# Kernel optimization log

Measured on AMD Instinct MI355X. Metric: run time of the kernel, lower is better.

## Reference

```python
import jax, jax.numpy as jnp
import numpy as np

N1, E1 = 50000, 400000   # drug graph nodes/edges
N2, E2 = 50000, 400000   # second-branch nodes/edges
G = 256                   # number of graphs in the batch
F1, F2 = 93, 43           # node feature dims


def setup_inputs() -> dict:
    key = jax.random.key(0)
    ks = jax.random.split(key, 40)
    rn = lambda k, s, sc=0.05: jax.random.normal(k, s, dtype=jnp.float32) * sc
    inp = {}
    inp["data"] = 0  # unused placeholder arg in the original forward
    inp["x"] = jax.random.normal(ks[0], (N1, F1), dtype=jnp.float32)
    inp["edge_index"] = jax.random.randint(ks[1], (2, E1), 0, N1)
    inp["batch"] = jnp.sort(jax.random.randint(ks[2], (N1,), 0, G))
    inp["a"] = jax.random.normal(ks[3], (N2, F2), dtype=jnp.float32)
    inp["edge"] = jax.random.randint(ks[4], (2, E2), 0, N2)
    inp["c"] = jnp.sort(jax.random.randint(ks[5], (N2,), 0, G))
    # GINConv linear weights (x @ W + b convention)
    inp["W1"] = rn(ks[6], (F1, F1));        inp["b1"] = rn(ks[7], (F1,))
    inp["W2"] = rn(ks[8], (F1, F1 * 10));   inp["b2"] = rn(ks[9], (F1 * 10,))
    inp["W3"] = rn(ks[10], (F2, F2));       inp["b3"] = rn(ks[11], (F2,))
    inp["W4"] = rn(ks[12], (F2, F2 * 10));  inp["b4"] = rn(ks[13], (F2 * 10,))
    # fc_g: 1860 -> 1024 -> 512 ; fc_g1: 860 -> 1024 -> 512
    inp["fcg_w1"] = rn(ks[14], (F1 * 10 * 2, 1024)); inp["fcg_b1"] = rn(ks[15], (1024,))
    inp["fcg_w2"] = rn(ks[16], (1024, 512));         inp["fcg_b2"] = rn(ks[17], (512,))
    inp["fcg1_w1"] = rn(ks[18], (F2 * 10 * 2, 1024)); inp["fcg1_b1"] = rn(ks[19], (1024,))
    inp["fcg1_w2"] = rn(ks[20], (1024, 512));         inp["fcg1_b2"] = rn(ks[21], (512,))
    # fc_final / fc_final1: 512 -> 256 -> 1
    inp["ff_w1"] = rn(ks[22], (512, 256)); inp["ff_b1"] = rn(ks[23], (256,))
    inp["ff_w2"] = rn(ks[24], (256, 1));   inp["ff_b2"] = rn(ks[25], (1,))
    inp["ff1_w1"] = rn(ks[26], (512, 256)); inp["ff1_b1"] = rn(ks[27], (256,))
    inp["ff1_w2"] = rn(ks[28], (256, 1));   inp["ff1_b2"] = rn(ks[29], (1,))
    return inp


def _gin(h, ei, W, b):
    # PyG GINConv(eps=0): Linear(x_i + sum_{j->i} x_j)
    agg = jax.ops.segment_sum(h[ei[0]], ei[1], num_segments=h.shape[0])
    return (h + agg) @ W + b


def _pool(h, seg):
    # concat(global_max_pool, global_mean_pool) per graph -> [G, 2*d]
    s = jax.ops.segment_sum(h, seg, num_segments=G)
    cnt = jax.ops.segment_sum(jnp.ones((h.shape[0], 1), h.dtype), seg, num_segments=G)
    mean = s / jnp.maximum(cnt, 1.0)
    mx = jax.ops.segment_max(h, seg, num_segments=G)
    mx = jnp.where(jnp.isfinite(mx), mx, 0.0)
    return jnp.concatenate([mx, mean], axis=1)


def reference(data, x, edge_index, batch, a, edge, c,
              W1, b1, W2, b2, W3, b3, W4, b4,
              fcg_w1, fcg_b1, fcg_w2, fcg_b2,
              fcg1_w1, fcg1_b1, fcg1_w2, fcg1_b2,
              ff_w1, ff_b1, ff_w2, ff_b2,
              ff1_w1, ff1_b1, ff1_w2, ff1_b2):
    relu = jax.nn.relu
    # branch 1 (93-dim features)
    h = relu(_gin(x, edge_index, W1, b1))
    h = relu(_gin(h, edge_index, W2, b2))          # [N1, 930]
    p = _pool(h, batch)                             # [G, 1860]
    x_g = relu(p @ fcg_w1 + fcg_b1) @ fcg_w2 + fcg_b2   # [G, 512] (dropout = identity at eval)
    z = relu(x_g @ ff_w1 + ff_b1) @ ff_w2 + ff_b2        # [G, 1]
    # branch 2 (43-dim features)
    h1 = relu(_gin(a, edge, W3, b3))
    h1 = relu(_gin(h1, edge, W4, b4))               # [N2, 430]
    p1 = _pool(h1, c)                                # [G, 860]
    x_g1 = relu(p1 @ fcg1_w1 + fcg1_b1) @ fcg1_w2 + fcg1_b2  # [G, 512]
    z1 = relu(x_g1 @ ff1_w1 + ff1_b1) @ ff1_w2 + ff1_b2       # [G, 1]
    return (z, x_g, x_g1, z1)
```

## Files before the change

### kernel.cpp

```cpp
#include <hip/hip_runtime.h>


static constexpr int NG  = 256;
static constexpr int CHK = 4096;

typedef short  short8  __attribute__((ext_vector_type(8)));
typedef float  floatx4 __attribute__((ext_vector_type(4)));

__device__ __forceinline__ short f2bf(float f) {
    unsigned u = __float_as_uint(f);
    u += 0x7fff + ((u >> 16) & 1);
    return (short)(u >> 16);
}
__device__ __forceinline__ float bf_lo(unsigned u) { return __uint_as_float(u << 16); }
__device__ __forceinline__ float bf_hi(unsigned u) { return __uint_as_float(u & 0xffff0000u); }

static inline int cdiv(int a, int b) { return (a + b - 1) / b; }

__global__ void offs_both_kernel(const int* __restrict__ s1, int n1, int* __restrict__ o1,
                                 const int* __restrict__ s2, int n2, int* __restrict__ o2) {
    int t = blockIdx.x * 256 + threadIdx.x;
    int br = t >> 9;
    int g = t & 511;
    if (br > 1 || g > NG) return;
    const int* seg = br ? s2 : s1;
    int N = br ? n2 : n1;
    int* offs = br ? o2 : o1;
    int lo = 0, hi = N;
    while (lo < hi) {
        int mid = (lo + hi) >> 1;
        if (seg[mid] < g) lo = mid + 1; else hi = mid;
    }
    offs[g] = lo;
}

__device__ __forceinline__ void deg_win_dev(const int* __restrict__ ei, int E, int N,
                                            int* __restrict__ deg, int bid) {
    int win = bid & 7, chunk = bid >> 3;
    int e0 = chunk * CHK;
    int e1 = e0 + CHK; if (e1 > E) e1 = E;
    int wlo = (int)((long)win * N / 8);
    int whi = (int)((long)(win + 1) * N / 8);
    for (int e = e0 + threadIdx.x; e < e1; e += 256) {
        int dst = ei[E + e];
        if (dst >= wlo && dst < whi) atomicAdd(&deg[dst], 1);
    }
}

__global__ __launch_bounds__(256) void deg_win_both_kernel(
        const int* ei1, int E1, int N1, int* d1, int nblk1,
        const int* ei2, int E2, int N2, int* d2) {
    int bid = blockIdx.x;
    if (bid < nblk1) deg_win_dev(ei1, E1, N1, d1, bid);
    else             deg_win_dev(ei2, E2, N2, d2, bid - nblk1);
}

__global__ __launch_bounds__(256) void scan1_both_kernel(
        const int* __restrict__ d1, int N1, int* __restrict__ x1, int* __restrict__ bs1, int nb1,
        const int* __restrict__ d2, int N2, int* __restrict__ x2, int* __restrict__ bs2) {
    __shared__ int sh[256];
    const int* deg; int* excl; int* bsum; int N; int blk;
    if ((int)blockIdx.x < nb1) { deg = d1; excl = x1; bsum = bs1; N = N1; blk = blockIdx.x; }
    else { deg = d2; excl = x2; bsum = bs2; N = N2; blk = blockIdx.x - nb1; }
    int base = blk * 1024;
    int t = threadIdx.x;
    int v[4];
    int s = 0;
    #pragma unroll
    for (int i = 0; i < 4; ++i) {
        int idx = base + t * 4 + i;
        v[i] = s;
        s += (idx < N) ? deg[idx] : 0;
    }
    sh[t] = s;
    __syncthreads();
    for (int off = 1; off < 256; off <<= 1) {
        int xv = (t >= off) ? sh[t - off] : 0;
        __syncthreads();
        sh[t] += xv;
        __syncthreads();
    }
    int texcl = (t > 0) ? sh[t - 1] : 0;
    #pragma unroll
    for (int i = 0; i < 4; ++i) {
        int idx = base + t * 4 + i;
        if (idx < N) excl[idx] = texcl + v[i];
    }
    if (t == 255) bsum[blk] = sh[255];
}

__global__ void scan2_both_kernel(int* __restrict__ b1, int nb1,
                                  int* __restrict__ b2, int nb2) {
    if (threadIdx.x) return;
    int* b = blockIdx.x ? b2 : b1;
    int nb = blockIdx.x ? nb2 : nb1;
    int acc = 0;
    for (int i = 0; i < nb; ++i) { int t = b[i]; b[i] = acc; acc += t; }
}

__global__ void scan3_both_kernel(int* __restrict__ x1, const int* __restrict__ bs1,
                                  int* __restrict__ c1, int N1, int Ev1,
                                  int* __restrict__ x2, const int* __restrict__ bs2,
                                  int* __restrict__ c2, int N2, int Ev2, int nc1) {
    int bid = blockIdx.x;
    int* excl; const int* bsum; int* cur; int N, E, i;
    if (bid < nc1) { i = bid * 256 + threadIdx.x; excl = x1; bsum = bs1; cur = c1; N = N1; E = Ev1; }
    else { i = (bid - nc1) * 256 + threadIdx.x; excl = x2; bsum = bs2; cur = c2; N = N2; E = Ev2; }
    if (i < N) {
        int v = excl[i] + bsum[i >> 10];
        excl[i] = v;
        cur[i] = v;
    }
    if (i == 0) excl[N] = E;
}

__device__ __forceinline__ void fill_win_dev(const int* __restrict__ ei, int E, int N,
                                             int* __restrict__ cursor, int* __restrict__ csr,
                                             int bid) {
    int win = bid & 7, chunk = bid >> 3;
    int e0 = chunk * CHK;
    int e1 = e0 + CHK; if (e1 > E) e1 = E;
    int wlo = (int)((long)win * N / 8);
    int whi = (int)((long)(win + 1) * N / 8);
    for (int e = e0 + threadIdx.x; e < e1; e += 256) {
        int dst = ei[E + e];
        if (dst >= wlo && dst < whi) {
            int pos = atomicAdd(&cursor[dst], 1);
            csr[pos] = ei[e];
        }
    }
}

__global__ __launch_bounds__(256) void fill_win_both_kernel(
        const int* ei1, int E1, int N1, int* c1, int* s1, int nblk1,
        const int* ei2, int E2, int N2, int* c2, int* s2) {
    int bid = blockIdx.x;
    if (bid < nblk1) fill_win_dev(ei1, E1, N1, c1, s1, bid);
    else             fill_win_dev(ei2, E2, N2, c2, s2, bid - nblk1);
}

struct RJob { const float* W; short* Wb; int K, Nsrc, Ndst, KP; };
struct RJobs10 { RJob j[10]; };

__global__ __launch_bounds__(256) void repack_all_kernel(RJobs10 jobs) {
    __shared__ __align__(16) short sh[64][72];
    RJob jb = jobs.j[blockIdx.y];
    int tilesC = (jb.Ndst + 63) >> 6;
    int tilesK = (jb.KP + 63) >> 6;
    if ((int)blockIdx.x >= tilesC * tilesK) return;
    int c0 = ((int)blockIdx.x % tilesC) * 64;
    int k0 = ((int)blockIdx.x / tilesC) * 64;
    int t = threadIdx.x;
    #pragma unroll 4
    for (int idx = t; idx < 64 * 64; idx += 256) {
        int kk = idx >> 6, cc = idx & 63;
        int k = k0 + kk, cg = c0 + cc;
        float v = (k < jb.K && cg < jb.Nsrc) ? jb.W[(size_t)k * jb.Nsrc + cg] : 0.f;
        sh[cc][kk] = f2bf(v);
    }
    __syncthreads();
    int kt = jb.KP - k0; if (kt > 64) kt = 64;
    int chunks = kt >> 3;
    for (int idx = t; idx < 64 * chunks; idx += 256) {
        int cc = idx / chunks, ch = idx - cc * chunks;
        int cg = c0 + cc;
        if (cg < jb.Ndst) {
            uint4 v = *(const uint4*)&sh[cc][ch * 8];
            *(uint4*)&jb.Wb[(size_t)cg * jb.KP + k0 + ch * 8] = v;
        }
    }
}

__global__ __launch_bounds__(256) void cast_both_kernel(
        const float* __restrict__ x1, unsigned short* __restrict__ xb1, int N1,
        const float* __restrict__ x2, unsigned short* __restrict__ xb2, int N2) {
    int idx = blockIdx.x * 256 + threadIdx.x;
    int tot1 = N1 * 96;
    if (idx < tot1) {
        int n = idx / 96, k = idx - n * 96;
        float v = (k < 93) ? x1[(size_t)n * 93 + k] : 0.f;
        xb1[idx] = (unsigned short)f2bf(v);
    } else {
        idx -= tot1;
        if (idx < N2 * 48) {
            int n = idx / 48, k = idx - n * 48;
            float v = (k < 43) ? x2[(size_t)n * 43 + k] : 0.f;
            xb2[idx] = (unsigned short)f2bf(v);
        }
    }
}

template<int FP, int GROUPS>
__device__ __forceinline__ void gather_dev(
        const unsigned short* __restrict__ src, const int* __restrict__ csr,
        const int* __restrict__ ro, unsigned short* __restrict__ vb, int N, int bid) {
    int wave = (bid * 256 + threadIdx.x) >> 6;
    int lane = threadIdx.x & 63;
    if (wave >= N) return;
    constexpr int HW = FP / 2;
    const unsigned* base = (const unsigned*)src;
    unsigned* out = (unsigned*)vb;
    int s = ro[wave], e = ro[wave + 1];
    int grp, l;
    if (GROUPS == 2) { grp = lane >> 5; l = lane & 31; }
    else             { grp = 0;         l = lane;      }
    bool act = l < HW;
    unsigned su = (act && grp == 0) ? base[(size_t)wave * HW + l] : 0u;
    float lo = bf_lo(su), hi = bf_hi(su);
    int i = s + grp;
    if (GROUPS == 1) {
        for (; i + 7 < e; i += 8) {
            unsigned u[8];
            #pragma unroll
            for (int q = 0; q < 8; ++q)
                u[q] = act ? base[(size_t)csr[i + q] * HW + l] : 0u;
            #pragma unroll
            for (int q = 0; q < 8; ++q) { lo += bf_lo(u[q]); hi += bf_hi(u[q]); }
        }
        for (; i < e; ++i) {
            unsigned u0 = act ? base[(size_t)csr[i] * HW + l] : 0u;
            lo += bf_lo(u0); hi += bf_hi(u0);
        }
    } else {
        for (; i + 6 < e; i += 8) {
            unsigned u[4];
            #pragma unroll
            for (int q = 0; q < 4; ++q)
                u[q] = act ? base[(size_t)csr[i + 2 * q] * HW + l] : 0u;
            #pragma unroll
            for (int q = 0; q < 4; ++q) { lo += bf_lo(u[q]); hi += bf_hi(u[q]); }
        }
        for (; i < e; i += 2) {
            unsigned u0 = act ? base[(size_t)csr[i] * HW + l] : 0u;
            lo += bf_lo(u0); hi += bf_hi(u0);
        }
        lo += __shfl_xor(lo, 32, 64);
        hi += __shfl_xor(hi, 32, 64);
    }
    if (grp == 0 && act) {
        unsigned plo = (unsigned)(unsigned short)f2bf(lo);
        unsigned phi = (unsigned)(unsigned short)f2bf(hi);
        out[(size_t)wave * HW + l] = (phi << 16) | plo;
    }
}

__global__ __launch_bounds__(256) void gather_both_kernel(
        const unsigned short* s1, const int* csr1, const int* ro1,
        unsigned short* vb1, int N1, int nblk1,
        const unsigned short* s2, const int* csr2, const int* ro2,
        unsigned short* vb2, int N2) {
    int bid = blockIdx.x;
    if (bid < nblk1) gather_dev<96, 1>(s1, csr1, ro1, vb1, N1, bid);
    else             gather_dev<48, 2>(s2, csr2, ro2, vb2, N2, bid - nblk1);
}

template<int FP, int KP, int KK>
__device__ __forceinline__ void load_afr(const short* __restrict__ vr,
                                         int row0, int ln, int quad,
                                         short8 afr[][4]) {
    #pragma unroll
    for (int ms = 0; ms < 4; ++ms) {
        const short* rp = vr + (size_t)(row0 + ms * 16 + ln) * FP;
        #pragma unroll
        for (int kk = 0; kk < KK; ++kk) {
            int offk = kk * 32 + quad * 8;
            short8 v = {0, 0, 0, 0, 0, 0, 0, 0};
            if (FP == KP || offk + 8 <= FP)
                v = *(const short8*)(rp + offk);
            afr[kk][ms] = v;
        }
    }
}

template<int F, int KP, int NT, int FP>
__device__ __forceinline__ void gin_linear_dev(
        const unsigned short* __restrict__ vb, const short* __restrict__ Wb,
        const float* __restrict__ b, unsigned short* __restrict__ h1b,
        int N, int blk) {
    constexpr int KK = KP / 32;
    int c0 = blk * 64;
    int tid = threadIdx.x;
    int wid = tid >> 6;
    int lane = tid & 63;
    int ln = lane & 15, quad = lane >> 4;
    int cvalid = N - c0; if (cvalid > 64) cvalid = 64;
    const short* vr = (const short*)vb;
    short8 afr[KK][4];
    load_afr<FP, KP, KK>(vr, c0, ln, quad, afr);
    for (int nt = wid; nt < NT; nt += 4) {
        int col = nt * 16 + ln;
        float bcol = (col < F) ? b[col] : 0.f;
        short8 bfr[KK];
        const short8* bp = (const short8*)(Wb + (size_t)col * KP + quad * 8);
        #pragma unroll
        for (int kk = 0; kk < KK; ++kk) bfr[kk] = bp[kk * 4];
        #pragma unroll
        for (int ms = 0; ms < 4; ++ms) {
            if (ms * 16 < cvalid) {
                floatx4 acc = {0.f, 0.f, 0.f, 0.f};
                #pragma unroll
                for (int kk = 0; kk < KK; ++kk)
                    acc = __builtin_amdgcn_mfma_f32_16x16x32_bf16(
                              afr[kk][ms], bfr[kk], acc, 0, 0, 0);
                #pragma unroll
                for (int r = 0; r < 4; ++r) {
                    int row = ms * 16 + quad * 4 + r;
                    if (row < cvalid) {
                        unsigned short hv = 0;
                        if (col < F) hv = (unsigned short)f2bf(fmaxf(acc[r] + bcol, 0.f));
                        h1b[(size_t)(c0 + row) * FP + col] = hv;
                    }
                }
            }
        }
    }
}

__global__ __launch_bounds__(256) void gin_linear_both_kernel(
        const unsigned short* vb1, const short* Wbl1, const float* bb1,
        unsigned short* h1b1, int N1, int nblk1,
        const unsigned short* vb2, const short* Wbl2, const float* bb2,
        unsigned short* h1b2, int N2) {
    int bid = blockIdx.x;
    if (bid < nblk1)
        gin_linear_dev<93, 96, 6, 96>(vb1, Wbl1, bb1, h1b1, N1, bid);
    else
        gin_linear_dev<43, 64, 3, 48>(vb2, Wbl2, bb2, h1b2, N2, bid - nblk1);
}

template<int F, int KP, int FO, int NT, int NS, int FP>
__device__ __forceinline__ void gin_pool_dev(
        const unsigned short* __restrict__ vb, const short* __restrict__ Wb,
        const float* __restrict__ b, const int* __restrict__ offs,
        float* __restrict__ ppmax, float* __restrict__ ppsum,
        int blk, float* pmaxL, float* psumL) {
    constexpr int KK = KP / 32;
    int g = blk / NS;
    int s = blk % NS;
    int tid = threadIdx.x;
    int wid = tid >> 6;
    int lane = tid & 63;
    int ln = lane & 15;
    int quad = lane >> 4;

    int gs0 = offs[g], ge0 = offs[g + 1];
    int per = (ge0 - gs0 + NS - 1) / NS;
    int gs = gs0 + s * per;
    int ge = gs + per; if (ge > ge0) ge = ge0;

    for (int i = tid; i < NT * 16; i += 256) { pmaxL[i] = 0.f; psumL[i] = 0.f; }
    __syncthreads();

    const short* vr = (const short*)vb;
    for (int c0 = gs; c0 < ge; c0 += 64) {
        int cvalid = ge - c0; if (cvalid > 64) cvalid = 64;
        short8 afr[KK][4];
        load_afr<FP, KP, KK>(vr, c0, ln, quad, afr);
        for (int nt = wid; nt < NT; nt += 4) {
            int col = nt * 16 + ln;
            float bcol = (col < FO) ? b[col] : 0.f;
            short8 bfr[KK];
            const short8* bp = (const short8*)(Wb + (size_t)col * KP + quad * 8);
            #pragma unroll
            for (int kk = 0; kk < KK; ++kk) bfr[kk] = bp[kk * 4];
            float cmx = 0.f, csm = 0.f;
            #pragma unroll
            for (int ms = 0; ms < 4; ++ms) {
                if (ms * 16 < cvalid) {
                    floatx4 acc = {0.f, 0.f, 0.f, 0.f};
                    #pragma unroll
                    for (int kk = 0; kk < KK; ++kk)
                        acc = __builtin_amdgcn_mfma_f32_16x16x32_bf16(
                                  afr[kk][ms], bfr[kk], acc, 0, 0, 0);
                    #pragma unroll
                    for (int r = 0; r < 4; ++r) {
                        int rowl = ms * 16 + quad * 4 + r;
                        float v = fmaxf(acc[r] + bcol, 0.f);
                        if (rowl < cvalid) { cmx = fmaxf(cmx, v); csm += v; }
                    }
                }
            }
            cmx = fmaxf(cmx, __shfl_xor(cmx, 16, 64));
            cmx = fmaxf(cmx, __shfl_xor(cmx, 32, 64));
            csm += __shfl_xor(csm, 16, 64);
            csm += __shfl_xor(csm, 32, 64);
            if (quad == 0) {
                int i = nt * 16 + ln;
                pmaxL[i] = fmaxf(pmaxL[i], cmx);
                psumL[i] += csm;
            }
        }
    }
    __syncthreads();
    float* om = ppmax + (size_t)(g * NS + s) * FO;
    float* os = ppsum + (size_t)(g * NS + s) * FO;
    for (int col = tid; col < FO; col += 256) { om[col] = pmaxL[col]; os[col] = psumL[col]; }
}

__global__ __launch_bounds__(256) void gin_pool_both_kernel(
        const unsigned short* vb1, const short* Wbg1, const float* b21,
        const int* offs1, float* pm1, float* ps1, int nblk1,
        const unsigned short* vb2, const short* Wbg2, const float* b22,
        const int* offs2, float* pm2, float* ps2) {
    __shared__ float pmaxL[944];
    __shared__ float psumL[944];
    int bid = blockIdx.x;
    if (bid < nblk1)
        gin_pool_dev<93, 96, 930, 59, 4, 96>(vb1, Wbg1, b21, offs1,
                                             pm1, ps1, bid, pmaxL, psumL);
    else
        gin_pool_dev<43, 64, 430, 27, 4, 48>(vb2, Wbg2, b22, offs2,
                                             pm2, ps2, bid - nblk1, pmaxL, psumL);
}

template<int FO, int NS, int KPAD>
__device__ __forceinline__ void pool_reduce_dev(
        const float* __restrict__ ppmax, const float* __restrict__ ppsum,
        const int* __restrict__ offs, short* __restrict__ pb, int g) {
    int cntg = offs[g + 1] - offs[g];
    float den = (float)(cntg > 0 ? cntg : 1);
    for (int col = threadIdx.x; col < KPAD; col += 256) {
        float v = 0.f;
        if (col < FO) {
            float m = 0.f;
            #pragma unroll
            for (int ss = 0; ss < NS; ++ss)
                m = fmaxf(m, ppmax[(size_t)(g * NS + ss) * FO + col]);
            v = m;
        } else if (col < 2 * FO) {
            float sm = 0.f;
            #pragma unroll
            for (int ss = 0; ss < NS; ++ss)
                sm += ppsum[(size_t)(g * NS + ss) * FO + (col - FO)];
            v = sm / den;
        }
        pb[(size_t)g * KPAD + col] = f2bf(v);
    }
}

__global__ __launch_bounds__(256) void pool_reduce_both_kernel(
        const float* pm1, const float* ps1, const int* offs1, short* pb1,
        const float* pm2, const float* ps2, const int* offs2, short* pb2) {
    int bid = blockIdx.x;
    if (bid < NG) pool_reduce_dev<930, 4, 2048>(pm1, ps1, offs1, pb1, bid);
    else          pool_reduce_dev<430, 4, 1024>(pm2, ps2, offs2, pb2, bid - NG);
}

template<int KPC>
__device__ __forceinline__ void fc_mfma_dev(
        const short* __restrict__ Ab, const short* __restrict__ Wb,
        float* __restrict__ partial, int KP, int NB, int bid) {
    int mb = bid & 3;
    int nb = (bid >> 2) % NB;
    int ks = (bid >> 2) / NB;
    int tid = threadIdx.x;
    int w = tid >> 6;
    int lane = tid & 63;
    int ln = lane & 15, quad = lane >> 4;
    int row = mb * 64 + w * 16 + ln;
    const short* ap = Ab + (size_t)row * KP + ks * KPC + quad * 8;
    const short* wp = Wb + (size_t)(nb * 64 + ln) * KP + ks * KPC + quad * 8;
    floatx4 acc[4];
    #pragma unroll
    for (int ns = 0; ns < 4; ++ns) acc[ns] = {0.f, 0.f, 0.f, 0.f};
    #pragma unroll
    for (int kk = 0; kk < KPC / 32; ++kk) {
        short8 a = *(const short8*)(ap + kk * 32);
        #pragma unroll
        for (int ns = 0; ns < 4; ++ns) {
            short8 b = *(const short8*)(wp + (size_t)ns * 16 * KP + kk * 32);
            acc[ns] = __builtin_amdgcn_mfma_f32_16x16x32_bf16(a, b, acc[ns], 0, 0, 0);
        }
    }
    int N = NB * 64;
    float* pp = partial + ((size_t)ks * 256 + mb * 64 + w * 16) * N + nb * 64;
    #pragma unroll
    for (int ns = 0; ns < 4; ++ns)
        #pragma unroll
        for (int r = 0; r < 4; ++r)
            pp[(quad * 4 + r) * N + ns * 16 + ln] = acc[ns][r];
}

template<int KPC1, int KPC2>
__global__ __launch_bounds__(256) void fc_mfma_both_kernel(
        const short* A1, const short* B1, float* P1, int KPa, int NBa, int nblk1,
        const short* A2, const short* B2, float* P2, int KPb, int NBb) {
    int bid = blockIdx.x;
    if (bid < nblk1) fc_mfma_dev<KPC1>(A1, B1, P1, KPa, NBa, bid);
    else             fc_mfma_dev<KPC2>(A2, B2, P2, KPb, NBb, bid - nblk1);
}

template<int KS, bool RELU, bool WBF16, bool WF32>
__global__ __launch_bounds__(256) void fc_reduce_both_kernel(
        const float* __restrict__ P1, const float* __restrict__ b1v,
        short* __restrict__ ob1, float* __restrict__ of1, int MN1, int Nn1,
        const float* __restrict__ P2, const float* __restrict__ b2v,
        short* __restrict__ ob2, float* __restrict__ of2, int MN2, int Nn2) {
    int idx = blockIdx.x * 256 + threadIdx.x;
    const float* P; const float* bias; short* ob; float* of; int MN, Nn;
    if (idx < MN1) { P = P1; bias = b1v; ob = ob1; of = of1; MN = MN1; Nn = Nn1; }
    else {
        idx -= MN1;
        if (idx >= MN2) return;
        P = P2; bias = b2v; ob = ob2; of = of2; MN = MN2; Nn = Nn2;
    }
    float v = bias[idx % Nn];
    #pragma unroll
    for (int s = 0; s < KS; ++s) v += P[(size_t)s * MN + idx];
    if (RELU) v = fmaxf(v, 0.f);
    if (WBF16) ob[idx] = f2bf(v);
    if (WF32)  of[idx] = v;
}

template<int KS>
__global__ __launch_bounds__(256) void head_final_both_kernel(
        const float* __restrict__ P1, const float* __restrict__ b11,
        const float* __restrict__ w21, const float* __restrict__ b21,
        float* __restrict__ z1o,
        const float* __restrict__ P2, const float* __restrict__ b12,
        const float* __restrict__ w22, const float* __restrict__ b22,
        float* __restrict__ z2o) {
    int br = blockIdx.x >> 8;
    int row = blockIdx.x & 255;
    const float* P  = br ? P2  : P1;
    const float* b1 = br ? b12 : b11;
    const float* w2 = br ? w22 : w21;
    const float* b2 = br ? b22 : b21;
    float* zo       = br ? z2o : z1o;
    int t = threadIdx.x;
    float v = b1[t];
    int idx = row * 256 + t;
    #pragma unroll
    for (int s = 0; s < KS; ++s) v += P[(size_t)s * 65536 + idx];
    v = fmaxf(v, 0.f) * w2[t];
    #pragma unroll
    for (int o = 32; o > 0; o >>= 1) v += __shfl_down(v, o, 64);
    __shared__ float red[4];
    if ((t & 63) == 0) red[t >> 6] = v;
    __syncthreads();
    if (t == 0) zo[row] = red[0] + red[1] + red[2] + red[3] + b2[0];
}

extern "C" void kernel_launch(void* const* d_in, const int* in_sizes, int n_in,
                              void* d_out, int out_size, void* d_ws, size_t ws_size,
                              hipStream_t stream) {
    (void)n_in; (void)out_size; (void)ws_size;
    const float* x      = (const float*)d_in[1];
    const int*   ei     = (const int*)  d_in[2];
    const int*   batch  = (const int*)  d_in[3];
    const float* a      = (const float*)d_in[4];
    const int*   ed     = (const int*)  d_in[5];
    const int*   c      = (const int*)  d_in[6];
    const float* W1  = (const float*)d_in[7],  *b1  = (const float*)d_in[8];
    const float* W2  = (const float*)d_in[9],  *b2  = (const float*)d_in[10];
    const float* W3  = (const float*)d_in[11], *b3  = (const float*)d_in[12];
    const float* W4  = (const float*)d_in[13], *b4  = (const float*)d_in[14];
    const float* fg_w1  = (const float*)d_in[15], *fg_b1  = (const float*)d_in[16];
    const float* fg_w2  = (const float*)d_in[17], *fg_b2  = (const float*)d_in[18];
    const float* fg1_w1 = (const float*)d_in[19], *fg1_b1 = (const float*)d_in[20];
    const float* fg1_w2 = (const float*)d_in[21], *fg1_b2 = (const float*)d_in[22];
    const float* ff_w1  = (const float*)d_in[23], *ff_b1  = (const float*)d_in[24];
    const float* ff_w2  = (const float*)d_in[25], *ff_b2  = (const float*)d_in[26];
    const float* ff1_w1 = (const float*)d_in[27], *ff1_b1 = (const float*)d_in[28];
    const float* ff1_w2 = (const float*)d_in[29], *ff1_b2 = (const float*)d_in[30];

    const int N1 = in_sizes[1] / 93;
    const int E1 = in_sizes[2] / 2;
    const int N2 = in_sizes[4] / 43;
    const int E2 = in_sizes[5] / 2;

    float* out = (float*)d_out;
    float* z   = out;
    float* xg  = out + 256;
    float* xg1 = out + 256 + 256 * 512;
    float* z1  = out + 256 + 2 * 256 * 512;

    char* wsb = (char*)d_ws;
    size_t off = 0;
    auto carve = [&](size_t bytes) {
        void* ptr = wsb + off;
        off = (off + bytes + 255) & ~(size_t)255;
        return ptr;
    };
    unsigned short* xb1  = (unsigned short*)carve((size_t)N1 * 96 * 2);
    unsigned short* xb2  = (unsigned short*)carve((size_t)N2 * 48 * 2);
    unsigned short* vb1  = (unsigned short*)carve((size_t)(N1 + 64) * 96 * 2);
    unsigned short* vb2  = (unsigned short*)carve((size_t)(N2 + 64) * 48 * 2);
    unsigned short* h1b1 = (unsigned short*)carve((size_t)N1 * 96 * 2);
    unsigned short* h1b2 = (unsigned short*)carve((size_t)N2 * 48 * 2);
    short* pb1  = (short*)carve((size_t)NG * 2048 * 2);
    short* pb2  = (short*)carve((size_t)NG * 1024 * 2);
    short* t1b1 = (short*)carve((size_t)NG * 1024 * 2);
    short* t1b2 = (short*)carve((size_t)NG * 1024 * 2);
    short* xgb1 = (short*)carve((size_t)NG * 512 * 2);
    short* xgb2 = (short*)carve((size_t)NG * 512 * 2);
    float* partial1 = (float*)carve((size_t)8 * 256 * 1024 * 4);
    float* partial2 = (float*)carve((size_t)8 * 256 * 1024 * 4);
    short* Wbl1 = (short*)carve((size_t)96 * 96 * 2);
    short* Wbg1 = (short*)carve((size_t)944 * 96 * 2);
    short* Wbl2 = (short*)carve((size_t)48 * 64 * 2);
    short* Wbg2 = (short*)carve((size_t)432 * 64 * 2);
    short* Wb1a = (short*)carve((size_t)1024 * 2048 * 2);
    short* Wb2a = (short*)carve((size_t)512 * 1024 * 2);
    short* Wb3a = (short*)carve((size_t)256 * 512 * 2);
    short* Wb1b = (short*)carve((size_t)1024 * 1024 * 2);
    short* Wb2b = (short*)carve((size_t)512 * 1024 * 2);
    short* Wb3b = (short*)carve((size_t)256 * 512 * 2);
    int* offs1 = (int*)carve(257 * 4);
    int* offs2 = (int*)carve(257 * 4);
    int* deg   = (int*)carve((size_t)(N1 + N2) * 4);
    int* rowoff1 = (int*)carve((size_t)(N1 + 1) * 4);
    int* rowoff2 = (int*)carve((size_t)(N2 + 1) * 4);
    int* cursor1 = (int*)carve((size_t)N1 * 4);
    int* cursor2 = (int*)carve((size_t)N2 * 4);
    int* csr1  = (int*)carve((size_t)E1 * 4);
    int* csr2  = (int*)carve((size_t)E2 * 4);
    int* bsum  = (int*)carve(256 * 4);
    int* deg1 = deg, *deg2 = deg + N1;
    int* bsum1 = bsum, *bsum2 = bsum + 128;
    float* pm1 = (float*)xb1;
    float* ps1 = pm1 + (size_t)NG * 4 * 930;
    float* pm2 = (float*)xb2;
    float* ps2 = pm2 + (size_t)NG * 4 * 430;

    constexpr int KS = 8;

    RJobs10 jobs = {{
        { W1,     Wbl1, 93,   93,   96,   96   },
        { W2,     Wbg1, 93,   930,  944,  96   },
        { W3,     Wbl2, 43,   43,   48,   64   },
        { W4,     Wbg2, 43,   430,  432,  64   },
        { fg_w1,  Wb1a, 1860, 1024, 1024, 2048 },
        { fg_w2,  Wb2a, 1024, 512,  512,  1024 },
        { ff_w1,  Wb3a, 512,  256,  256,  512  },
        { fg1_w1, Wb1b, 860,  1024, 1024, 1024 },
        { fg1_w2, Wb2b, 1024, 512,  512,  1024 },
        { ff1_w1, Wb3b, 512,  256,  256,  512  },
    }};
    repack_all_kernel<<<dim3(512, 10), 256, 0, stream>>>(jobs);
    cast_both_kernel<<<cdiv(N1 * 96 + N2 * 48, 256), 256, 0, stream>>>(
        x, xb1, N1, a, xb2, N2);
    offs_both_kernel<<<4, 256, 0, stream>>>(batch, N1, offs1, c, N2, offs2);
    hipMemsetAsync(deg, 0, (size_t)(N1 + N2) * 4, stream);
    int nwb1 = cdiv(E1, CHK) * 8, nwb2 = cdiv(E2, CHK) * 8;
    deg_win_both_kernel<<<nwb1 + nwb2, 256, 0, stream>>>(ei, E1, N1, deg1, nwb1,
                                                         ed, E2, N2, deg2);
    int nb1 = cdiv(N1, 1024), nb2 = cdiv(N2, 1024);
    scan1_both_kernel<<<nb1 + nb2, 256, 0, stream>>>(deg1, N1, rowoff1, bsum1, nb1,
                                                     deg2, N2, rowoff2, bsum2);
    scan2_both_kernel<<<2, 64, 0, stream>>>(bsum1, nb1, bsum2, nb2);
    int nc1 = cdiv(N1, 256), nc2 = cdiv(N2, 256);
    scan3_both_kernel<<<nc1 + nc2, 256, 0, stream>>>(rowoff1, bsum1, cursor1, N1, E1,
                                                     rowoff2, bsum2, cursor2, N2, E2, nc1);
    fill_win_both_kernel<<<nwb1 + nwb2, 256, 0, stream>>>(ei, E1, N1, cursor1, csr1, nwb1,
                                                          ed, E2, N2, cursor2, csr2);

    int ng1 = cdiv(N1, 4), ng2 = cdiv(N2, 4);
    gather_both_kernel<<<ng1 + ng2, 256, 0, stream>>>(
        xb1, csr1, rowoff1, vb1, N1, ng1, xb2, csr2, rowoff2, vb2, N2);
    int nl1 = cdiv(N1, 64), nl2 = cdiv(N2, 64);
    gin_linear_both_kernel<<<nl1 + nl2, 256, 0, stream>>>(
        vb1, Wbl1, b1, h1b1, N1, nl1, vb2, Wbl2, b3, h1b2, N2);
    gather_both_kernel<<<ng1 + ng2, 256, 0, stream>>>(
        h1b1, csr1, rowoff1, vb1, N1, ng1, h1b2, csr2, rowoff2, vb2, N2);
    gin_pool_both_kernel<<<NG * 4 * 2, 256, 0, stream>>>(
        vb1, Wbg1, b2, offs1, pm1, ps1, NG * 4,
        vb2, Wbg2, b4, offs2, pm2, ps2);
    pool_reduce_both_kernel<<<2 * NG, 256, 0, stream>>>(
        pm1, ps1, offs1, pb1, pm2, ps2, offs2, pb2);

    fc_mfma_both_kernel<256, 128><<<1024, 256, 0, stream>>>(
        pb1, Wb1a, partial1, 2048, 16, 512, pb2, Wb1b, partial2, 1024, 16);
    fc_reduce_both_kernel<KS, true, true, false><<<cdiv(2 * 256 * 1024, 256), 256, 0, stream>>>(
        partial1, fg_b1, t1b1, nullptr, 256 * 1024, 1024,
        partial2, fg1_b1, t1b2, nullptr, 256 * 1024, 1024);
    fc_mfma_both_kernel<128, 128><<<512, 256, 0, stream>>>(
        t1b1, Wb2a, partial1, 1024, 8, 256, t1b2, Wb2b, partial2, 1024, 8);
    fc_reduce_both_kernel<KS, false, true, true><<<cdiv(2 * 256 * 512, 256), 256, 0, stream>>>(
        partial1, fg_b2, xgb1, xg, 256 * 512, 512,
        partial2, fg1_b2, xgb2, xg1, 256 * 512, 512);
    fc_mfma_both_kernel<64, 64><<<256, 256, 0, stream>>>(
        xgb1, Wb3a, partial1, 512, 4, 128, xgb2, Wb3b, partial2, 512, 4);
    head_final_both_kernel<KS><<<512, 256, 0, stream>>>(
        partial1, ff_b1, ff_w2, ff_b2, z,
        partial2, ff1_b1, ff1_w2, ff1_b2, z1);
}
```

Before: 454.1 us.

## Fuse prologue kernels, pad branch-2 features to 64, and merge gather tail loops

```diff
diff --git a/kernel.cpp b/kernel.cpp
--- a/kernel.cpp
+++ b/kernel.cpp
@@ -17,21 +17,43 @@
 
 static inline int cdiv(int a, int b) { return (a + b - 1) / b; }
 
-__global__ void offs_both_kernel(const int* __restrict__ s1, int n1, int* __restrict__ o1,
-                                 const int* __restrict__ s2, int n2, int* __restrict__ o2) {
-    int t = blockIdx.x * 256 + threadIdx.x;
-    int br = t >> 9;
-    int g = t & 511;
-    if (br > 1 || g > NG) return;
-    const int* seg = br ? s2 : s1;
-    int N = br ? n2 : n1;
-    int* offs = br ? o2 : o1;
-    int lo = 0, hi = N;
-    while (lo < hi) {
-        int mid = (lo + hi) >> 1;
-        if (seg[mid] < g) lo = mid + 1; else hi = mid;
-    }
-    offs[g] = lo;
+__global__ __launch_bounds__(256) void prologue_kernel(
+        const float* __restrict__ x1, unsigned short* __restrict__ xb1, int N1,
+        const float* __restrict__ x2, unsigned short* __restrict__ xb2, int N2,
+        const int* __restrict__ seg1, int* __restrict__ offs1,
+        const int* __restrict__ seg2, int* __restrict__ offs2,
+        int* __restrict__ deg, int castB1, int castB2, int degB) {
+    int b = blockIdx.x;
+    int t = threadIdx.x;
+    if (b < castB1) {
+        int idx = b * 256 + t;
+        if (idx < N1 * 96) {
+            int n = idx / 96, k = idx - n * 96;
+            xb1[idx] = (unsigned short)f2bf(k < 93 ? x1[(size_t)n * 93 + k] : 0.f);
+        }
+    } else if (b < castB1 + castB2) {
+        int idx = (b - castB1) * 256 + t;
+        if (idx < N2 * 64) {
+            int n = idx >> 6, k = idx & 63;
+            xb2[idx] = (unsigned short)f2bf(k < 43 ? x2[(size_t)n * 43 + k] : 0.f);
+        }
+    } else if (b < castB1 + castB2 + degB) {
+        int idx = (b - castB1 - castB2) * 256 + t;
+        if (idx < N1 + N2) deg[idx] = 0;
+    } else {
+        int br = b - castB1 - castB2 - degB;
+        const int* seg = br ? seg2 : seg1;
+        int N = br ? N2 : N1;
+        int* offs = br ? offs2 : offs1;
+        for (int g = t; g <= NG; g += 256) {
+            int lo = 0, hi = N;
+            while (lo < hi) {
+                int mid = (lo + hi) >> 1;
+                if (seg[mid] < g) lo = mid + 1; else hi = mid;
+            }
+            offs[g] = lo;
+        }
+    }
 }
 
 __device__ __forceinline__ void deg_win_dev(const int* __restrict__ ei, int E, int N,
@@ -167,25 +189,6 @@
         if (cg < jb.Ndst) {
             uint4 v = *(const uint4*)&sh[cc][ch * 8];
             *(uint4*)&jb.Wb[(size_t)cg * jb.KP + k0 + ch * 8] = v;
-        }
-    }
-}
-
-__global__ __launch_bounds__(256) void cast_both_kernel(
-        const float* __restrict__ x1, unsigned short* __restrict__ xb1, int N1,
-        const float* __restrict__ x2, unsigned short* __restrict__ xb2, int N2) {
-    int idx = blockIdx.x * 256 + threadIdx.x;
-    int tot1 = N1 * 96;
-    if (idx < tot1) {
-        int n = idx / 96, k = idx - n * 96;
-        float v = (k < 93) ? x1[(size_t)n * 93 + k] : 0.f;
-        xb1[idx] = (unsigned short)f2bf(v);
-    } else {
-        idx -= tot1;
-        if (idx < N2 * 48) {
-            int n = idx / 48, k = idx - n * 48;
-            float v = (k < 43) ? x2[(size_t)n * 43 + k] : 0.f;
-            xb2[idx] = (unsigned short)f2bf(v);
         }
     }
 }
@@ -207,32 +210,31 @@
     bool act = l < HW;
     unsigned su = (act && grp == 0) ? base[(size_t)wave * HW + l] : 0u;
     float lo = bf_lo(su), hi = bf_hi(su);
-    int i = s + grp;
     if (GROUPS == 1) {
-        for (; i + 7 < e; i += 8) {
+        for (int i = s; i < e; i += 8) {
             unsigned u[8];
             #pragma unroll
+            for (int q = 0; q < 8; ++q) {
+                int j = i + q;
+                int jj = j < e ? j : e - 1;
+                u[q] = act ? base[(size_t)csr[jj] * HW + l] : 0u;
+            }
+            #pragma unroll
             for (int q = 0; q < 8; ++q)
-                u[q] = act ? base[(size_t)csr[i + q] * HW + l] : 0u;
-            #pragma unroll
-            for (int q = 0; q < 8; ++q) { lo += bf_lo(u[q]); hi += bf_hi(u[q]); }
-        }
-        for (; i < e; ++i) {
-            unsigned u0 = act ? base[(size_t)csr[i] * HW + l] : 0u;
-            lo += bf_lo(u0); hi += bf_hi(u0);
+                if (i + q < e) { lo += bf_lo(u[q]); hi += bf_hi(u[q]); }
         }
     } else {
-        for (; i + 6 < e; i += 8) {
+        for (int i = s + grp; i < e; i += 8) {
             unsigned u[4];
             #pragma unroll
+            for (int q = 0; q < 4; ++q) {
+                int j = i + 2 * q;
+                int jj = j < e ? j : e - 1;
+                u[q] = act ? base[(size_t)csr[jj] * HW + l] : 0u;
+            }
+            #pragma unroll
             for (int q = 0; q < 4; ++q)
-                u[q] = act ? base[(size_t)csr[i + 2 * q] * HW + l] : 0u;
-            #pragma unroll
-            for (int q = 0; q < 4; ++q) { lo += bf_lo(u[q]); hi += bf_hi(u[q]); }
-        }
-        for (; i < e; i += 2) {
-            unsigned u0 = act ? base[(size_t)csr[i] * HW + l] : 0u;
-            lo += bf_lo(u0); hi += bf_hi(u0);
+                if (i + 2 * q < e) { lo += bf_lo(u[q]); hi += bf_hi(u[q]); }
         }
         lo += __shfl_xor(lo, 32, 64);
         hi += __shfl_xor(hi, 32, 64);
@@ -251,7 +253,7 @@
         unsigned short* vb2, int N2) {
     int bid = blockIdx.x;
     if (bid < nblk1) gather_dev<96, 1>(s1, csr1, ro1, vb1, N1, bid);
-    else             gather_dev<48, 2>(s2, csr2, ro2, vb2, N2, bid - nblk1);
+    else             gather_dev<64, 2>(s2, csr2, ro2, vb2, N2, bid - nblk1);
 }
 
 template<int FP, int KP, int KK>
@@ -308,7 +310,8 @@
                     if (row < cvalid) {
                         unsigned short hv = 0;
                         if (col < F) hv = (unsigned short)f2bf(fmaxf(acc[r] + bcol, 0.f));
-                        h1b[(size_t)(c0 + row) * FP + col] = hv;
+                        if (col < FP)
+                            h1b[(size_t)(c0 + row) * FP + col] = hv;
                     }
                 }
             }
@@ -325,7 +328,7 @@
     if (bid < nblk1)
         gin_linear_dev<93, 96, 6, 96>(vb1, Wbl1, bb1, h1b1, N1, bid);
     else
-        gin_linear_dev<43, 64, 3, 48>(vb2, Wbl2, bb2, h1b2, N2, bid - nblk1);
+        gin_linear_dev<43, 64, 4, 64>(vb2, Wbl2, bb2, h1b2, N2, bid - nblk1);
 }
 
 template<int F, int KP, int FO, int NT, int NS, int FP>
@@ -409,7 +412,7 @@
         gin_pool_dev<93, 96, 930, 59, 4, 96>(vb1, Wbg1, b21, offs1,
                                              pm1, ps1, bid, pmaxL, psumL);
     else
-        gin_pool_dev<43, 64, 430, 27, 4, 48>(vb2, Wbg2, b22, offs2,
+        gin_pool_dev<43, 64, 430, 27, 4, 64>(vb2, Wbg2, b22, offs2,
                                              pm2, ps2, bid - nblk1, pmaxL, psumL);
 }
 
@@ -583,11 +586,11 @@
         return ptr;
     };
     unsigned short* xb1  = (unsigned short*)carve((size_t)N1 * 96 * 2);
-    unsigned short* xb2  = (unsigned short*)carve((size_t)N2 * 48 * 2);
+    unsigned short* xb2  = (unsigned short*)carve((size_t)N2 * 64 * 2);
     unsigned short* vb1  = (unsigned short*)carve((size_t)(N1 + 64) * 96 * 2);
-    unsigned short* vb2  = (unsigned short*)carve((size_t)(N2 + 64) * 48 * 2);
+    unsigned short* vb2  = (unsigned short*)carve((size_t)(N2 + 64) * 64 * 2);
     unsigned short* h1b1 = (unsigned short*)carve((size_t)N1 * 96 * 2);
-    unsigned short* h1b2 = (unsigned short*)carve((size_t)N2 * 48 * 2);
+    unsigned short* h1b2 = (unsigned short*)carve((size_t)N2 * 64 * 2);
     short* pb1  = (short*)carve((size_t)NG * 2048 * 2);
     short* pb2  = (short*)carve((size_t)NG * 1024 * 2);
     short* t1b1 = (short*)carve((size_t)NG * 1024 * 2);
@@ -598,7 +601,7 @@
     float* partial2 = (float*)carve((size_t)8 * 256 * 1024 * 4);
     short* Wbl1 = (short*)carve((size_t)96 * 96 * 2);
     short* Wbg1 = (short*)carve((size_t)944 * 96 * 2);
-    short* Wbl2 = (short*)carve((size_t)48 * 64 * 2);
+    short* Wbl2 = (short*)carve((size_t)64 * 64 * 2);
     short* Wbg2 = (short*)carve((size_t)432 * 64 * 2);
     short* Wb1a = (short*)carve((size_t)1024 * 2048 * 2);
     short* Wb2a = (short*)carve((size_t)512 * 1024 * 2);
@@ -628,7 +631,7 @@
     RJobs10 jobs = {{
         { W1,     Wbl1, 93,   93,   96,   96   },
         { W2,     Wbg1, 93,   930,  944,  96   },
-        { W3,     Wbl2, 43,   43,   48,   64   },
+        { W3,     Wbl2, 43,   43,   64,   64   },
         { W4,     Wbg2, 43,   430,  432,  64   },
         { fg_w1,  Wb1a, 1860, 1024, 1024, 2048 },
         { fg_w2,  Wb2a, 1024, 512,  512,  1024 },
@@ -638,10 +641,10 @@
         { ff1_w1, Wb3b, 512,  256,  256,  512  },
     }};
     repack_all_kernel<<<dim3(512, 10), 256, 0, stream>>>(jobs);
-    cast_both_kernel<<<cdiv(N1 * 96 + N2 * 48, 256), 256, 0, stream>>>(
-        x, xb1, N1, a, xb2, N2);
-    offs_both_kernel<<<4, 256, 0, stream>>>(batch, N1, offs1, c, N2, offs2);
-    hipMemsetAsync(deg, 0, (size_t)(N1 + N2) * 4, stream);
+    int castB1 = cdiv(N1 * 96, 256), castB2 = cdiv(N2 * 64, 256);
+    int degB = cdiv(N1 + N2, 256);
+    prologue_kernel<<<castB1 + castB2 + degB + 2, 256, 0, stream>>>(
+        x, xb1, N1, a, xb2, N2, batch, offs1, c, offs2, deg, castB1, castB2, degB);
     int nwb1 = cdiv(E1, CHK) * 8, nwb2 = cdiv(E2, CHK) * 8;
     deg_win_both_kernel<<<nwb1 + nwb2, 256, 0, stream>>>(ei, E1, N1, deg1, nwb1,
                                                          ed, E2, N2, deg2);
```

Result: no change. 453.2 us (-0.2%).
